# Optimization experiments

Hardware: AMD Instinct MI355X
Metric: run time of the kernel (lower is better)

## Reference

```python
import jax, jax.numpy as jnp
import numpy as np

N_AGENTS = 12
N_THREADS = 4096
DIM = 3
N_VEC = 4
HID = 64
INV_NF = 32
LAYERS = 2
N = N_THREADS * N_AGENTS


def _intra_graph_edges():
    # fully-connected directed edges within each env's agent graph
    i, j = np.meshgrid(np.arange(N_AGENTS), np.arange(N_AGENTS), indexing='ij')
    mask = i != j
    ri, ci = i[mask], j[mask]  # [132]
    off = (np.arange(N_THREADS) * N_AGENTS)[:, None]
    row = (ri[None, :] + off).reshape(-1).astype(np.int32)
    col = (ci[None, :] + off).reshape(-1).astype(np.int32)
    return jnp.asarray(row), jnp.asarray(col)


def setup_inputs() -> dict:
    key = jax.random.key(0)
    ks = jax.random.split(key, 16)
    s = 0.05
    row, col = _intra_graph_edges()
    return {
        'h0': jax.random.normal(ks[0], (N, INV_NF), jnp.float32),
        'x0': jax.random.normal(ks[1], (N, DIM, N_VEC), jnp.float32),
        'W_embed': jax.random.normal(ks[2], (INV_NF, HID), jnp.float32) * s,
        'b_embed': jnp.zeros((HID,), jnp.float32),
        'We1': jax.random.normal(ks[3], (LAYERS, 2 * HID + N_VEC, HID), jnp.float32) * s,
        'be1': jnp.zeros((LAYERS, HID), jnp.float32),
        'We2': jax.random.normal(ks[4], (LAYERS, HID, HID), jnp.float32) * s,
        'be2': jnp.zeros((LAYERS, HID), jnp.float32),
        'Wx': jax.random.normal(ks[5], (LAYERS, HID, N_VEC), jnp.float32) * s,
        'bx': jnp.zeros((LAYERS, N_VEC), jnp.float32),
        'Wh1': jax.random.normal(ks[6], (LAYERS, 2 * HID, HID), jnp.float32) * s,
        'bh1': jnp.zeros((LAYERS, HID), jnp.float32),
        'Wh2': jax.random.normal(ks[7], (LAYERS, HID, HID), jnp.float32) * s,
        'bh2': jnp.zeros((LAYERS, HID), jnp.float32),
        'w_act': jax.random.normal(ks[8], (N_VEC,), jnp.float32) * s,
        'log_std': jnp.full((DIM,), -0.5, jnp.float32),
        'row': row,
        'col': col,
    }


def reference(h0, x0, W_embed, b_embed, We1, be1, We2, be2, Wx, bx,
              Wh1, bh1, Wh2, bh2, w_act, log_std, row, col):
    silu = jax.nn.silu
    n = h0.shape[0]
    h = h0 @ W_embed + b_embed            # node embedding, [N, HID]
    x = x0                                 # equivariant features, [N, DIM, N_VEC]
    deg = jnp.maximum(jax.ops.segment_sum(jnp.ones_like(row, jnp.float32), row, num_segments=n), 1.0)
    for l in range(LAYERS):
        hi, hj = h[row], h[col]
        diff = x[row] - x[col]                        # [E, DIM, N_VEC]
        radial = jnp.sum(diff * diff, axis=1)          # [E, N_VEC]
        m = silu(jnp.concatenate([hi, hj, radial], -1) @ We1[l] + be1[l])
        m = silu(m @ We2[l] + be2[l])                  # edge messages [E, HID]
        wc = m @ Wx[l] + bx[l]                         # per-vector coord weights [E, N_VEC]
        x = x + jax.ops.segment_sum(diff * wc[:, None, :], row, num_segments=n) / deg[:, None, None]
        agg = jax.ops.segment_sum(m, row, num_segments=n)
        h = h + silu(jnp.concatenate([h, agg], -1) @ Wh1[l] + bh1[l]) @ Wh2[l] + bh2[l]
    mu = jnp.einsum('ndv,v->nd', x, w_act)             # act_net: Linear(N_VEC,1,bias=False)
    actions = mu                                        # deterministic: mode of Normal(mu, std)
    log_probs = jnp.broadcast_to(-log_std - 0.5 * jnp.log(2.0 * jnp.pi), mu.shape)
    actions = actions.reshape(N_THREADS, N_AGENTS, DIM)
    log_probs = log_probs.reshape(N_THREADS, N_AGENTS, DIM)
    return actions, log_probs
```

## Files before the change

### kernel.cpp

```cpp
#include <hip/hip_runtime.h>

#define NAG 12
#define NTH 4096
#define NEDGE 132
#define LDB 72
#define LDT 20

typedef __bf16 bf16_8 __attribute__((ext_vector_type(8)));
typedef __bf16 bf16_4 __attribute__((ext_vector_type(4)));
typedef float  f32x4  __attribute__((ext_vector_type(4)));

#define MFMA(a,b,c) __builtin_amdgcn_mfma_f32_16x16x32_bf16((a),(b),(c),0,0,0)

#define WS_FRAGS 100
#define WS_BIAS_F32 25600
#define WS_BX_F32   27648
#define WS_BYTES 111104

__device__ __forceinline__ float silu_f(float z) {
    float e = __expf(-z);
    return z * __builtin_amdgcn_rcpf(1.0f + e);
}

__device__ __forceinline__ bf16_8 loadB64(const float* __restrict__ W, int kbase, int n, int q) {
    bf16_8 b;
    #pragma unroll
    for (int j = 0; j < 8; ++j) b[j] = (__bf16)W[(kbase + q*8 + j) * 64 + n];
    return b;
}

__device__ __forceinline__ bf16_8 packA8(const float* S) {
    f32x4 u = *(const f32x4*)S, v = *(const f32x4*)(S + 4);
    bf16_8 a;
    a[0]=(__bf16)u.x; a[1]=(__bf16)u.y; a[2]=(__bf16)u.z; a[3]=(__bf16)u.w;
    a[4]=(__bf16)v.x; a[5]=(__bf16)v.y; a[6]=(__bf16)v.z; a[7]=(__bf16)v.w;
    return a;
}

__global__ __launch_bounds__(64) void prep_frags(
    const float* __restrict__ W_embed, const float* __restrict__ We1,
    const float* __restrict__ We2, const float* __restrict__ Wh1,
    const float* __restrict__ Wh2,
    const float* __restrict__ be1, const float* __restrict__ be2,
    const float* __restrict__ bh1, const float* __restrict__ bh2,
    const float* __restrict__ bx, __bf16* __restrict__ wsb)
{
    const int f = blockIdx.x, lane = threadIdx.x;
    const int q = lane >> 4, n16 = lane & 15;
    float* wsf = (float*)wsb;
    if (f < WS_FRAGS) {
        const float* src; int kbase, nbase;
        if (f < 4) { src = W_embed; kbase = 0; nbase = f * 16; }
        else {
            int g0 = f - 4, l = g0 / 48, r = g0 % 48;
            if      (r < 8)  { int nt=r>>1, kh=r&1;            src = We1 + l*NEDGE*64; kbase = kh*32;      nbase = nt*16; }
            else if (r < 16) { int rr=r-8,  nt=rr>>1, kh=rr&1; src = We1 + l*NEDGE*64; kbase = 64 + kh*32; nbase = nt*16; }
            else if (r < 24) { int rr=r-16, nt=rr>>1, kh=rr&1; src = We2 + l*64*64;    kbase = kh*32;      nbase = nt*16; }
            else if (r < 40) { int rr=r-24, nt=rr>>2, ks=rr&3; src = Wh1 + l*128*64;   kbase = ks*32;      nbase = nt*16; }
            else             { int rr=r-40, nt=rr>>1, kh=rr&1; src = Wh2 + l*64*64;    kbase = kh*32;      nbase = nt*16; }
        }
        bf16_8 b = loadB64(src, kbase, nbase + n16, q);
        *(bf16_8*)(wsb + (size_t)f * 512 + lane * 8) = b;
    } else if (f < WS_FRAGS + 8) {
        int f2 = f - WS_FRAGS, l = f2 >> 2, w = f2 & 3;
        const float* src = (w == 0 ? be1 : w == 1 ? be2 : w == 2 ? bh1 : bh2) + l * 64;
        f32x4 v = { src[n16], src[16 + n16], src[32 + n16], src[48 + n16] };
        *(f32x4*)(wsf + WS_BIAS_F32 + ((size_t)(l*4 + w) * 64 + lane) * 4) = v;
    } else {
        #pragma unroll
        for (int l = 0; l < 2; ++l)
            wsf[WS_BX_F32 + l*64 + lane] = (n16 < 4) ? bx[l*4 + n16] : 0.f;
    }
}

template<bool WS>
__device__ __forceinline__ bf16_8 frg(const __bf16* __restrict__ wsb, int fid,
                                      const float* __restrict__ src, int kbase, int n, int lane) {
    if (WS) return *(const bf16_8*)(wsb + (size_t)fid * 512 + lane * 8);
    else    return loadB64(src, kbase, n, (lane >> 4));
}

template<bool WS>
__global__ void __launch_bounds__(64) egnn9(
    const float* __restrict__ h0, const float* __restrict__ x0,
    const float* __restrict__ W_embed, const float* __restrict__ b_embed,
    const float* __restrict__ We1, const float* __restrict__ be1,
    const float* __restrict__ We2, const float* __restrict__ be2,
    const float* __restrict__ Wx, const float* __restrict__ bx,
    const float* __restrict__ Wh1, const float* __restrict__ bh1,
    const float* __restrict__ Wh2, const float* __restrict__ bh2,
    const float* __restrict__ w_act, const float* __restrict__ log_std,
    const __bf16* __restrict__ wsb, float* __restrict__ out)
{
    __shared__ __align__(16) __bf16 sh  [NAG * LDB];
    __shared__ __align__(16) __bf16 sHa [NAG * LDB];
    __shared__ __align__(16) __bf16 sHb [NAG * LDB];
    __shared__ __align__(16) __bf16 mstT[2][64 * LDT];
    __shared__ __align__(16) float  sx  [NAG * 16];
    __shared__ __align__(16) float  sRad[NEDGE * 4];
    __shared__ __align__(16) __bf16 sWcB[NEDGE * 4];
    __shared__ __align__(16) float  sWb [4 * 64];

    const int lane = threadIdx.x;
    const int q = lane >> 4, n16 = lane & 15;
    const int rowA = (n16 < NAG) ? n16 : (NAG - 1);
    const int env  = blockIdx.x;
    const float* wsf = (const float*)wsb;

    if (lane < NAG * 3) {
        int d = lane % 3;
        out[NTH * NAG * 3 + env * (NAG*3) + lane] = -log_std[d] - 0.9189385332046727f;
    }

    #pragma unroll
    for (int p = 0; p < 3; ++p) {
        int idx = p * 64 + lane;
        if (idx < NAG * 12) sx[(idx / 12) * 16 + idx % 12] = x0[env * NAG * 12 + idx];
    }

    f32x4 hC[4];
    {
        const float* hp = h0 + (env * NAG + rowA) * 32 + q * 8;
        bf16_8 a = packA8(hp);
        #pragma unroll
        for (int nt = 0; nt < 4; ++nt) {
            bf16_8 b = frg<WS>(wsb, nt, W_embed, 0, nt*16 + n16, lane);
            f32x4 acc = {0.f,0.f,0.f,0.f};
            acc = MFMA(a, b, acc);
            float bias = b_embed[nt*16 + n16];
            #pragma unroll
            for (int r = 0; r < 4; ++r) acc[r] += bias;
            hC[nt] = acc;
        }
        #pragma unroll
        for (int nt = 0; nt < 4; ++nt)
            #pragma unroll
            for (int r = 0; r < 4; ++r) {
                int row = q*4 + r;
                if (row < NAG) sh[row*LDB + nt*16 + n16] = (__bf16)hC[nt][r];
            }
    }

    #pragma unroll 1
    for (int l = 0; l < 2; ++l) {
        const float* We1l = We1 + l * NEDGE * 64;
        const float* be1l = be1 + l * 64;
        const float* be2l = be2 + l * 64;
        const float* Wxl  = Wx  + l * 64 * 4;
        const float* bxl  = bx  + l * 4;
        const float* We2l = We2 + l * 64 * 64;
        const float* Wh1l = Wh1 + l * 128 * 64;
        const float* bh1l = bh1 + l * 64;
        const float* Wh2l = Wh2 + l * 64 * 64;
        const float* bh2l = bh2 + l * 64;
        const int L = 4 + l * 48;

        f32x4 be1q, be2q, bh1q, bh2q;
        float bxv;
        if (WS) {
            const float* bb = wsf + WS_BIAS_F32 + (size_t)(l*4) * 256 + lane * 4;
            be1q = *(const f32x4*)(bb);
            be2q = *(const f32x4*)(bb + 256);
            bh1q = *(const f32x4*)(bb + 512);
            bh2q = *(const f32x4*)(bb + 768);
            bxv  = wsf[WS_BX_F32 + l*64 + lane];
        } else {
            #pragma unroll
            for (int nt = 0; nt < 4; ++nt) {
                be1q[nt] = be1l[nt*16+n16]; be2q[nt] = be2l[nt*16+n16];
                bh1q[nt] = bh1l[nt*16+n16]; bh2q[nt] = bh2l[nt*16+n16];
            }
            bxv = (n16 < 4) ? bxl[n16] : 0.f;
        }

        {
            bf16_8 a0 = *(const bf16_8*)(sh + rowA*LDB + q*8);
            bf16_8 a1 = *(const bf16_8*)(sh + rowA*LDB + 32 + q*8);
            #pragma unroll
            for (int nt = 0; nt < 4; ++nt) {
                bf16_8 b0 = frg<WS>(wsb, L+nt*2+0,   We1l, 0,  nt*16+n16, lane);
                bf16_8 b1 = frg<WS>(wsb, L+nt*2+1,   We1l, 32, nt*16+n16, lane);
                bf16_8 c0 = frg<WS>(wsb, L+8+nt*2+0, We1l, 64, nt*16+n16, lane);
                bf16_8 c1 = frg<WS>(wsb, L+8+nt*2+1, We1l, 96, nt*16+n16, lane);
                f32x4 aA = {0.f,0.f,0.f,0.f}, aB = {0.f,0.f,0.f,0.f};
                aA = MFMA(a0, b0, aA); aA = MFMA(a1, b1, aA);
                aB = MFMA(a0, c0, aB); aB = MFMA(a1, c1, aB);
                #pragma unroll
                for (int r = 0; r < 4; ++r) {
                    int row = q*4 + r;
                    if (row < NAG) {
                        sHa[row*LDB + nt*16+n16] = (__bf16)(aA[r] + be1q[nt]);
                        sHb[row*LDB + nt*16+n16] = (__bf16)aB[r];
                    }
                }
            }
        }
        #pragma unroll
        for (int p = 0; p < 4; ++p) sWb[p*64 + lane] = We1l[(128+p)*64 + lane];
        #pragma unroll
        for (int p = 0; p < 9; ++p) {
            int idx = p * 64 + lane;
            if (idx < NEDGE * 4) {
                int e = idx >> 2, v = idx & 3;
                int i = e / 11, jj = e - i * 11, j = jj + (jj >= i);
                float r = 0.f;
                #pragma unroll
                for (int d = 0; d < 3; ++d) {
                    float df = sx[i*16 + d*4 + v] - sx[j*16 + d*4 + v];
                    r += df * df;
                }
                sRad[idx] = r;
            }
        }

        float agg[NAG];
        #pragma unroll
        for (int i = 0; i < NAG; ++i) agg[i] = 0.f;
        bf16_8 w2f[4][2], wxf[2];
        #pragma unroll
        for (int nt = 0; nt < 4; ++nt) {
            w2f[nt][0] = frg<WS>(wsb, L+16+nt*2+0, We2l, 0,  nt*16+n16, lane);
            w2f[nt][1] = frg<WS>(wsb, L+16+nt*2+1, We2l, 32, nt*16+n16, lane);
        }
        #pragma unroll
        for (int kh = 0; kh < 2; ++kh) {
            bf16_8 b;
            #pragma unroll
            for (int j2 = 0; j2 < 8; ++j2)
                b[j2] = (n16 < 4) ? (__bf16)Wxl[(kh*32 + q*8 + j2)*4 + n16] : (__bf16)0.f;
            wxf[kh] = b;
        }

        #pragma unroll
        for (int t = 0; t < 9; ++t) {
            __bf16* mT = &mstT[t & 1][0];
            const int e  = t*16 + n16;
            const int ec = (e < NEDGE) ? e : (NEDGE - 1);
            const int i  = ec / 11;
            const int jj = ec - i * 11;
            const int j  = jj + (jj >= i);
            const f32x4 rd = *(const f32x4*)(sRad + ec * 4);
            bf16_8 af0, af1;
            #pragma unroll
            for (int kh = 0; kh < 2; ++kh) {
                const int cb = kh*32 + q*8;
                bf16_8 ha = *(const bf16_8*)(sHa + i*LDB + cb);
                bf16_8 hb = *(const bf16_8*)(sHb + j*LDB + cb);
                f32x4 wr0 = {0.f,0.f,0.f,0.f}, wr1 = {0.f,0.f,0.f,0.f};
                #pragma unroll
                for (int v = 0; v < 4; ++v) {
                    f32x4 wa = *(const f32x4*)(sWb + v*64 + cb);
                    f32x4 wb = *(const f32x4*)(sWb + v*64 + cb + 4);
                    wr0 += rd[v] * wa; wr1 += rd[v] * wb;
                }
                bf16_8 a;
                #pragma unroll
                for (int c = 0; c < 4; ++c)
                    a[c]   = (__bf16)silu_f((float)ha[c]   + (float)hb[c]   + wr0[c]);
                #pragma unroll
                for (int c = 0; c < 4; ++c)
                    a[4+c] = (__bf16)silu_f((float)ha[4+c] + (float)hb[4+c] + wr1[c]);
                if (kh == 0) af0 = a; else af1 = a;
            }
            #pragma unroll
            for (int nt = 0; nt < 4; ++nt) {
                f32x4 acc = {0.f,0.f,0.f,0.f};
                acc = MFMA(af0, w2f[nt][0], acc);
                acc = MFMA(af1, w2f[nt][1], acc);
                bf16_4 mv;
                #pragma unroll
                for (int r = 0; r < 4; ++r) mv[r] = (__bf16)silu_f(acc[r] + be2q[nt]);
                *(bf16_4*)(mT + (nt*16 + n16)*LDT + q*4) = mv;
            }
            {
                bf16_8 aw0, aw1;
                #pragma unroll
                for (int j2 = 0; j2 < 8; ++j2) {
                    aw0[j2] = mT[(q*8 + j2)*LDT + n16];
                    aw1[j2] = mT[(32 + q*8 + j2)*LDT + n16];
                }
                f32x4 acc = {0.f,0.f,0.f,0.f};
                acc = MFMA(aw0, wxf[0], acc);
                acc = MFMA(aw1, wxf[1], acc);
                if (n16 < 4) {
                    #pragma unroll
                    for (int r = 0; r < 4; ++r) {
                        int row = t*16 + q*4 + r;
                        if (row < NEDGE) sWcB[row*4 + n16] = (__bf16)(acc[r] + bxv);
                    }
                }
            }
            {
                bf16_4 c0 = *(const bf16_4*)(mT + lane*LDT + 0);
                #pragma unroll
                for (int el = 0; el < 4; ++el) agg[(t*16 + el)/11] += (float)c0[el];
                if (t < 8) {
                    bf16_4 c1 = *(const bf16_4*)(mT + lane*LDT + 4);
                    bf16_4 c2 = *(const bf16_4*)(mT + lane*LDT + 8);
                    bf16_4 c3 = *(const bf16_4*)(mT + lane*LDT + 12);
                    #pragma unroll
                    for (int el = 0; el < 4; ++el) {
                        agg[(t*16 + 4  + el)/11] += (float)c1[el];
                        agg[(t*16 + 8  + el)/11] += (float)c2[el];
                        agg[(t*16 + 12 + el)/11] += (float)c3[el];
                    }
                }
            }
        }
        #pragma unroll
        for (int i = 0; i < NAG; ++i) sHb[i*LDB + lane] = (__bf16)agg[i];

        float xn[3];
        #pragma unroll
        for (int p = 0; p < 3; ++p) {
            int idx = p*64 + lane;
            float res = 0.f;
            if (idx < 144) {
                int xi = idx / 12, dv = idx % 12, v = dv & 3;
                float xiv = sx[xi*16 + dv];
                float acc = 0.f;
                #pragma unroll
                for (int j2 = 0; j2 < NAG; ++j2) {
                    int e2 = xi*11 + j2 - (j2 > xi ? 1 : 0);
                    e2 = (e2 < NEDGE) ? e2 : (NEDGE - 1);
                    float term = (xiv - sx[j2*16 + dv]) * (float)sWcB[e2*4 + v];
                    acc += (j2 == xi) ? 0.f : term;
                }
                res = xiv + acc * (1.0f / 11.0f);
            }
            xn[p] = res;
        }
        {
            bf16_8 ah0 = *(const bf16_8*)(sh  + rowA*LDB + q*8);
            bf16_8 ah1 = *(const bf16_8*)(sh  + rowA*LDB + 32 + q*8);
            bf16_8 ag0 = *(const bf16_8*)(sHb + rowA*LDB + q*8);
            bf16_8 ag1 = *(const bf16_8*)(sHb + rowA*LDB + 32 + q*8);
            #pragma unroll
            for (int nt = 0; nt < 4; ++nt) {
                f32x4 acc = {0.f,0.f,0.f,0.f};
                acc = MFMA(ah0, frg<WS>(wsb, L+24+nt*4+0, Wh1l, 0,  nt*16+n16, lane), acc);
                acc = MFMA(ah1, frg<WS>(wsb, L+24+nt*4+1, Wh1l, 32, nt*16+n16, lane), acc);
                acc = MFMA(ag0, frg<WS>(wsb, L+24+nt*4+2, Wh1l, 64, nt*16+n16, lane), acc);
                acc = MFMA(ag1, frg<WS>(wsb, L+24+nt*4+3, Wh1l, 96, nt*16+n16, lane), acc);
                #pragma unroll
                for (int r = 0; r < 4; ++r) {
                    int row = q*4 + r;
                    if (row < NAG) sHa[row*LDB + nt*16+n16] = (__bf16)silu_f(acc[r] + bh1q[nt]);
                }
            }
        }
        #pragma unroll
        for (int p = 0; p < 3; ++p) {
            int idx = p*64 + lane;
            if (idx < 144) sx[(idx/12)*16 + idx%12] = xn[p];
        }
        {
            bf16_8 at0 = *(const bf16_8*)(sHa + rowA*LDB + q*8);
            bf16_8 at1 = *(const bf16_8*)(sHa + rowA*LDB + 32 + q*8);
            #pragma unroll
            for (int nt = 0; nt < 4; ++nt) {
                f32x4 acc = {0.f,0.f,0.f,0.f};
                acc = MFMA(at0, frg<WS>(wsb, L+40+nt*2+0, Wh2l, 0,  nt*16+n16, lane), acc);
                acc = MFMA(at1, frg<WS>(wsb, L+40+nt*2+1, Wh2l, 32, nt*16+n16, lane), acc);
                #pragma unroll
                for (int r = 0; r < 4; ++r) hC[nt][r] += acc[r] + bh2q[nt];
            }
            #pragma unroll
            for (int nt = 0; nt < 4; ++nt)
                #pragma unroll
                for (int r = 0; r < 4; ++r) {
                    int row = q*4 + r;
                    if (row < NAG) sh[row*LDB + nt*16+n16] = (__bf16)hC[nt][r];
                }
        }
    }

    if (lane < NAG * 3) {
        int i = lane / 3, d = lane - i * 3;
        float mu = 0.f;
        #pragma unroll
        for (int v = 0; v < 4; ++v) mu += sx[i*16 + d*4 + v] * w_act[v];
        out[env * (NAG*3) + lane] = mu;
    }
}

extern "C" void kernel_launch(void* const* d_in, const int* in_sizes, int n_in,
                              void* d_out, int out_size, void* d_ws, size_t ws_size,
                              hipStream_t stream) {
    const float* h0   = (const float*)d_in[0];
    const float* x0   = (const float*)d_in[1];
    const float* Wem  = (const float*)d_in[2];
    const float* bem  = (const float*)d_in[3];
    const float* We1  = (const float*)d_in[4];
    const float* be1  = (const float*)d_in[5];
    const float* We2  = (const float*)d_in[6];
    const float* be2  = (const float*)d_in[7];
    const float* Wx   = (const float*)d_in[8];
    const float* bx   = (const float*)d_in[9];
    const float* Wh1  = (const float*)d_in[10];
    const float* bh1  = (const float*)d_in[11];
    const float* Wh2  = (const float*)d_in[12];
    const float* bh2  = (const float*)d_in[13];
    const float* wact = (const float*)d_in[14];
    const float* lstd = (const float*)d_in[15];
    float* out = (float*)d_out;

    if (ws_size >= (size_t)WS_BYTES) {
        prep_frags<<<dim3(WS_FRAGS + 9), dim3(64), 0, stream>>>(
            Wem, We1, We2, Wh1, Wh2, be1, be2, bh1, bh2, bx, (__bf16*)d_ws);
        egnn9<true><<<dim3(NTH), dim3(64), 0, stream>>>(
            h0, x0, Wem, bem, We1, be1, We2, be2, Wx, bx,
            Wh1, bh1, Wh2, bh2, wact, lstd, (const __bf16*)d_ws, out);
    } else {
        egnn9<false><<<dim3(NTH), dim3(64), 0, stream>>>(
            h0, x0, Wem, bem, We1, be1, We2, be2, Wx, bx,
            Wh1, bh1, Wh2, bh2, wact, lstd, nullptr, out);
    }
}
```

Measured before the change: 239.6 us.

## Process two environments per wavefront to reuse weight fragments

Each 64-thread block now handles two environments instead of one, so the grid is halved. Each weight fragment loaded from the workspace or global memory feeds MFMAs for both environments, and the two independent MFMA chains can interleave for more instruction-level parallelism. In exchange, LDS use and register pressure per block roughly double (agg[2][12], hC[2][4]), which can lower occupancy or cause spills, and there are half as many blocks to spread across CUs.

```diff
diff --git a/kernel.cpp b/kernel.cpp
--- a/kernel.cpp
+++ b/kernel.cpp
@@ -81,7 +81,7 @@
 }
 
 template<bool WS>
-__global__ void __launch_bounds__(64) egnn9(
+__global__ void __launch_bounds__(64) egnn11(
     const float* __restrict__ h0, const float* __restrict__ x0,
     const float* __restrict__ W_embed, const float* __restrict__ b_embed,
     const float* __restrict__ We1, const float* __restrict__ be1,
@@ -92,53 +92,65 @@
     const float* __restrict__ w_act, const float* __restrict__ log_std,
     const __bf16* __restrict__ wsb, float* __restrict__ out)
 {
-    __shared__ __align__(16) __bf16 sh  [NAG * LDB];
-    __shared__ __align__(16) __bf16 sHa [NAG * LDB];
-    __shared__ __align__(16) __bf16 sHb [NAG * LDB];
-    __shared__ __align__(16) __bf16 mstT[2][64 * LDT];
-    __shared__ __align__(16) float  sx  [NAG * 16];
-    __shared__ __align__(16) float  sRad[NEDGE * 4];
-    __shared__ __align__(16) __bf16 sWcB[NEDGE * 4];
+    __shared__ __align__(16) __bf16 sh  [2][NAG * LDB];
+    __shared__ __align__(16) __bf16 sHa [2][NAG * LDB];
+    __shared__ __align__(16) __bf16 sHb [2][NAG * LDB];
+    __shared__ __align__(16) __bf16 mstT[2][2][64 * LDT];
+    __shared__ __align__(16) float  sx  [2][NAG * 16];
+    __shared__ __align__(16) float  sRad[2][NEDGE * 4];
+    __shared__ __align__(16) __bf16 sWcB[2][NEDGE * 4];
     __shared__ __align__(16) float  sWb [4 * 64];
 
     const int lane = threadIdx.x;
     const int q = lane >> 4, n16 = lane & 15;
     const int rowA = (n16 < NAG) ? n16 : (NAG - 1);
-    const int env  = blockIdx.x;
+    const int env0 = blockIdx.x * 2;
     const float* wsf = (const float*)wsb;
 
     if (lane < NAG * 3) {
         int d = lane % 3;
-        out[NTH * NAG * 3 + env * (NAG*3) + lane] = -log_std[d] - 0.9189385332046727f;
+        float lp = -log_std[d] - 0.9189385332046727f;
+        out[NTH * NAG * 3 + (env0 + 0) * (NAG*3) + lane] = lp;
+        out[NTH * NAG * 3 + (env0 + 1) * (NAG*3) + lane] = lp;
     }
 
     #pragma unroll
-    for (int p = 0; p < 3; ++p) {
+    for (int p = 0; p < 5; ++p) {
         int idx = p * 64 + lane;
-        if (idx < NAG * 12) sx[(idx / 12) * 16 + idx % 12] = x0[env * NAG * 12 + idx];
-    }
-
-    f32x4 hC[4];
+        if (idx < 2 * NAG * 12) {
+            int ep = idx / 144, r2 = idx - ep * 144;
+            sx[ep][(r2 / 12) * 16 + r2 % 12] = x0[(env0) * NAG * 12 + idx];
+        }
+    }
+
+    f32x4 hC[2][4];
     {
-        const float* hp = h0 + (env * NAG + rowA) * 32 + q * 8;
-        bf16_8 a = packA8(hp);
+        bf16_8 a[2];
+        #pragma unroll
+        for (int ep = 0; ep < 2; ++ep)
+            a[ep] = packA8(h0 + ((env0 + ep) * NAG + rowA) * 32 + q * 8);
         #pragma unroll
         for (int nt = 0; nt < 4; ++nt) {
             bf16_8 b = frg<WS>(wsb, nt, W_embed, 0, nt*16 + n16, lane);
-            f32x4 acc = {0.f,0.f,0.f,0.f};
-            acc = MFMA(a, b, acc);
             float bias = b_embed[nt*16 + n16];
             #pragma unroll
-            for (int r = 0; r < 4; ++r) acc[r] += bias;
-            hC[nt] = acc;
-        }
-        #pragma unroll
-        for (int nt = 0; nt < 4; ++nt)
-            #pragma unroll
-            for (int r = 0; r < 4; ++r) {
-                int row = q*4 + r;
-                if (row < NAG) sh[row*LDB + nt*16 + n16] = (__bf16)hC[nt][r];
-            }
+            for (int ep = 0; ep < 2; ++ep) {
+                f32x4 acc = {0.f,0.f,0.f,0.f};
+                acc = MFMA(a[ep], b, acc);
+                #pragma unroll
+                for (int r = 0; r < 4; ++r) acc[r] += bias;
+                hC[ep][nt] = acc;
+            }
+        }
+        #pragma unroll
+        for (int ep = 0; ep < 2; ++ep)
+            #pragma unroll
+            for (int nt = 0; nt < 4; ++nt)
+                #pragma unroll
+                for (int r = 0; r < 4; ++r) {
+                    int row = q*4 + r;
+                    if (row < NAG) sh[ep][row*LDB + nt*16 + n16] = (__bf16)hC[ep][nt][r];
+                }
     }
 
     #pragma unroll 1
@@ -174,23 +186,30 @@
         }
 
         {
-            bf16_8 a0 = *(const bf16_8*)(sh + rowA*LDB + q*8);
-            bf16_8 a1 = *(const bf16_8*)(sh + rowA*LDB + 32 + q*8);
+            bf16_8 a0[2], a1[2];
+            #pragma unroll
+            for (int ep = 0; ep < 2; ++ep) {
+                a0[ep] = *(const bf16_8*)(sh[ep] + rowA*LDB + q*8);
+                a1[ep] = *(const bf16_8*)(sh[ep] + rowA*LDB + 32 + q*8);
+            }
             #pragma unroll
             for (int nt = 0; nt < 4; ++nt) {
                 bf16_8 b0 = frg<WS>(wsb, L+nt*2+0,   We1l, 0,  nt*16+n16, lane);
                 bf16_8 b1 = frg<WS>(wsb, L+nt*2+1,   We1l, 32, nt*16+n16, lane);
                 bf16_8 c0 = frg<WS>(wsb, L+8+nt*2+0, We1l, 64, nt*16+n16, lane);
                 bf16_8 c1 = frg<WS>(wsb, L+8+nt*2+1, We1l, 96, nt*16+n16, lane);
-                f32x4 aA = {0.f,0.f,0.f,0.f}, aB = {0.f,0.f,0.f,0.f};
-                aA = MFMA(a0, b0, aA); aA = MFMA(a1, b1, aA);
-                aB = MFMA(a0, c0, aB); aB = MFMA(a1, c1, aB);
-                #pragma unroll
-                for (int r = 0; r < 4; ++r) {
-                    int row = q*4 + r;
-                    if (row < NAG) {
-                        sHa[row*LDB + nt*16+n16] = (__bf16)(aA[r] + be1q[nt]);
-                        sHb[row*LDB + nt*16+n16] = (__bf16)aB[r];
+                #pragma unroll
+                for (int ep = 0; ep < 2; ++ep) {
+                    f32x4 aA = {0.f,0.f,0.f,0.f}, aB = {0.f,0.f,0.f,0.f};
+                    aA = MFMA(a0[ep], b0, aA); aA = MFMA(a1[ep], b1, aA);
+                    aB = MFMA(a0[ep], c0, aB); aB = MFMA(a1[ep], c1, aB);
+                    #pragma unroll
+                    for (int r = 0; r < 4; ++r) {
+                        int row = q*4 + r;
+                        if (row < NAG) {
+                            sHa[ep][row*LDB + nt*16+n16] = (__bf16)(aA[r] + be1q[nt]);
+                            sHb[ep][row*LDB + nt*16+n16] = (__bf16)aB[r];
+                        }
                     }
                 }
             }
@@ -203,19 +222,24 @@
             if (idx < NEDGE * 4) {
                 int e = idx >> 2, v = idx & 3;
                 int i = e / 11, jj = e - i * 11, j = jj + (jj >= i);
-                float r = 0.f;
-                #pragma unroll
-                for (int d = 0; d < 3; ++d) {
-                    float df = sx[i*16 + d*4 + v] - sx[j*16 + d*4 + v];
-                    r += df * df;
-                }
-                sRad[idx] = r;
-            }
-        }
-
-        float agg[NAG];
-        #pragma unroll
-        for (int i = 0; i < NAG; ++i) agg[i] = 0.f;
+                #pragma unroll
+                for (int ep = 0; ep < 2; ++ep) {
+                    float r = 0.f;
+                    #pragma unroll
+                    for (int d = 0; d < 3; ++d) {
+                        float df = sx[ep][i*16 + d*4 + v] - sx[ep][j*16 + d*4 + v];
+                        r += df * df;
+                    }
+                    sRad[ep][idx] = r;
+                }
+            }
+        }
+
+        float agg[2][NAG];
+        #pragma unroll
+        for (int ep = 0; ep < 2; ++ep)
+            #pragma unroll
+            for (int i = 0; i < NAG; ++i) agg[ep][i] = 0.f;
         bf16_8 w2f[4][2], wxf[2];
         #pragma unroll
         for (int nt = 0; nt < 4; ++nt) {
@@ -233,46 +257,54 @@
 
         #pragma unroll
         for (int t = 0; t < 9; ++t) {
-            __bf16* mT = &mstT[t & 1][0];
             const int e  = t*16 + n16;
             const int ec = (e < NEDGE) ? e : (NEDGE - 1);
             const int i  = ec / 11;
             const int jj = ec - i * 11;
             const int j  = jj + (jj >= i);
-            const f32x4 rd = *(const f32x4*)(sRad + ec * 4);
-            bf16_8 af0, af1;
-            #pragma unroll
-            for (int kh = 0; kh < 2; ++kh) {
-                const int cb = kh*32 + q*8;
-                bf16_8 ha = *(const bf16_8*)(sHa + i*LDB + cb);
-                bf16_8 hb = *(const bf16_8*)(sHb + j*LDB + cb);
-                f32x4 wr0 = {0.f,0.f,0.f,0.f}, wr1 = {0.f,0.f,0.f,0.f};
-                #pragma unroll
-                for (int v = 0; v < 4; ++v) {
-                    f32x4 wa = *(const f32x4*)(sWb + v*64 + cb);
-                    f32x4 wb = *(const f32x4*)(sWb + v*64 + cb + 4);
-                    wr0 += rd[v] * wa; wr1 += rd[v] * wb;
-                }
-                bf16_8 a;
-                #pragma unroll
-                for (int c = 0; c < 4; ++c)
-                    a[c]   = (__bf16)silu_f((float)ha[c]   + (float)hb[c]   + wr0[c]);
-                #pragma unroll
-                for (int c = 0; c < 4; ++c)
-                    a[4+c] = (__bf16)silu_f((float)ha[4+c] + (float)hb[4+c] + wr1[c]);
-                if (kh == 0) af0 = a; else af1 = a;
-            }
-            #pragma unroll
-            for (int nt = 0; nt < 4; ++nt) {
-                f32x4 acc = {0.f,0.f,0.f,0.f};
-                acc = MFMA(af0, w2f[nt][0], acc);
-                acc = MFMA(af1, w2f[nt][1], acc);
-                bf16_4 mv;
-                #pragma unroll
-                for (int r = 0; r < 4; ++r) mv[r] = (__bf16)silu_f(acc[r] + be2q[nt]);
-                *(bf16_4*)(mT + (nt*16 + n16)*LDT + q*4) = mv;
-            }
-            {
+            bf16_8 af[2][2];
+            #pragma unroll
+            for (int ep = 0; ep < 2; ++ep) {
+                const f32x4 rd = *(const f32x4*)(sRad[ep] + ec * 4);
+                #pragma unroll
+                for (int kh = 0; kh < 2; ++kh) {
+                    const int cb = kh*32 + q*8;
+                    bf16_8 ha = *(const bf16_8*)(sHa[ep] + i*LDB + cb);
+                    bf16_8 hb = *(const bf16_8*)(sHb[ep] + j*LDB + cb);
+                    f32x4 wr0 = {0.f,0.f,0.f,0.f}, wr1 = {0.f,0.f,0.f,0.f};
+                    #pragma unroll
+                    for (int v = 0; v < 4; ++v) {
+                        f32x4 wa = *(const f32x4*)(sWb + v*64 + cb);
+                        f32x4 wb = *(const f32x4*)(sWb + v*64 + cb + 4);
+                        wr0 += rd[v] * wa; wr1 += rd[v] * wb;
+                    }
+                    bf16_8 a;
+                    #pragma unroll
+                    for (int c = 0; c < 4; ++c)
+                        a[c]   = (__bf16)silu_f((float)ha[c]   + (float)hb[c]   + wr0[c]);
+                    #pragma unroll
+                    for (int c = 0; c < 4; ++c)
+                        a[4+c] = (__bf16)silu_f((float)ha[4+c] + (float)hb[4+c] + wr1[c]);
+                    af[ep][kh] = a;
+                }
+            }
+            #pragma unroll
+            for (int ep = 0; ep < 2; ++ep) {
+                __bf16* mT = &mstT[ep][t & 1][0];
+                #pragma unroll
+                for (int nt = 0; nt < 4; ++nt) {
+                    f32x4 acc = {0.f,0.f,0.f,0.f};
+                    acc = MFMA(af[ep][0], w2f[nt][0], acc);
+                    acc = MFMA(af[ep][1], w2f[nt][1], acc);
+                    bf16_4 mv;
+                    #pragma unroll
+                    for (int r = 0; r < 4; ++r) mv[r] = (__bf16)silu_f(acc[r] + be2q[nt]);
+                    *(bf16_4*)(mT + (nt*16 + n16)*LDT + q*4) = mv;
+                }
+            }
+            #pragma unroll
+            for (int ep = 0; ep < 2; ++ep) {
+                const __bf16* mT = &mstT[ep][t & 1][0];
                 bf16_8 aw0, aw1;
                 #pragma unroll
                 for (int j2 = 0; j2 < 8; ++j2) {
@@ -286,101 +318,133 @@
                     #pragma unroll
                     for (int r = 0; r < 4; ++r) {
                         int row = t*16 + q*4 + r;
-                        if (row < NEDGE) sWcB[row*4 + n16] = (__bf16)(acc[r] + bxv);
-                    }
-                }
-            }
-            {
+                        if (row < NEDGE) sWcB[ep][row*4 + n16] = (__bf16)(acc[r] + bxv);
+                    }
+                }
+            }
+            #pragma unroll
+            for (int ep = 0; ep < 2; ++ep) {
+                const __bf16* mT = &mstT[ep][t & 1][0];
                 bf16_4 c0 = *(const bf16_4*)(mT + lane*LDT + 0);
                 #pragma unroll
-                for (int el = 0; el < 4; ++el) agg[(t*16 + el)/11] += (float)c0[el];
+                for (int el = 0; el < 4; ++el) agg[ep][(t*16 + el)/11] += (float)c0[el];
                 if (t < 8) {
                     bf16_4 c1 = *(const bf16_4*)(mT + lane*LDT + 4);
                     bf16_4 c2 = *(const bf16_4*)(mT + lane*LDT + 8);
                     bf16_4 c3 = *(const bf16_4*)(mT + lane*LDT + 12);
                     #pragma unroll
                     for (int el = 0; el < 4; ++el) {
-                        agg[(t*16 + 4  + el)/11] += (float)c1[el];
-                        agg[(t*16 + 8  + el)/11] += (float)c2[el];
-                        agg[(t*16 + 12 + el)/11] += (float)c3[el];
-                    }
-                }
-            }
-        }
-        #pragma unroll
-        for (int i = 0; i < NAG; ++i) sHb[i*LDB + lane] = (__bf16)agg[i];
-
-        float xn[3];
+                        agg[ep][(t*16 + 4  + el)/11] += (float)c1[el];
+                        agg[ep][(t*16 + 8  + el)/11] += (float)c2[el];
+                        agg[ep][(t*16 + 12 + el)/11] += (float)c3[el];
+                    }
+                }
+            }
+        }
+        #pragma unroll
+        for (int ep = 0; ep < 2; ++ep)
+            #pragma unroll
+            for (int i = 0; i < NAG; ++i) sHb[ep][i*LDB + lane] = (__bf16)agg[ep][i];
+
+        float xn[2][3];
         #pragma unroll
         for (int p = 0; p < 3; ++p) {
             int idx = p*64 + lane;
-            float res = 0.f;
-            if (idx < 144) {
-                int xi = idx / 12, dv = idx % 12, v = dv & 3;
-                float xiv = sx[xi*16 + dv];
+            int xi = idx / 12, dv = idx % 12, v = dv & 3;
+            bool act = idx < 144;
+            int xic = act ? xi : 0;
+            #pragma unroll
+            for (int ep = 0; ep < 2; ++ep) {
+                float xiv = sx[ep][xic*16 + dv];
                 float acc = 0.f;
                 #pragma unroll
                 for (int j2 = 0; j2 < NAG; ++j2) {
-                    int e2 = xi*11 + j2 - (j2 > xi ? 1 : 0);
+                    int e2 = xic*11 + j2 - (j2 > xic ? 1 : 0);
                     e2 = (e2 < NEDGE) ? e2 : (NEDGE - 1);
-                    float term = (xiv - sx[j2*16 + dv]) * (float)sWcB[e2*4 + v];
-                    acc += (j2 == xi) ? 0.f : term;
-                }
-                res = xiv + acc * (1.0f / 11.0f);
-            }
-            xn[p] = res;
+                    float term = (xiv - sx[ep][j2*16 + dv]) * (float)sWcB[ep][e2*4 + v];
+                    acc += (j2 == xic) ? 0.f : term;
+                }
+                xn[ep][p] = act ? (xiv + acc * (1.0f / 11.0f)) : 0.f;
+            }
         }
         {
-            bf16_8 ah0 = *(const bf16_8*)(sh  + rowA*LDB + q*8);
-            bf16_8 ah1 = *(const bf16_8*)(sh  + rowA*LDB + 32 + q*8);
-            bf16_8 ag0 = *(const bf16_8*)(sHb + rowA*LDB + q*8);
-            bf16_8 ag1 = *(const bf16_8*)(sHb + rowA*LDB + 32 + q*8);
+            bf16_8 ah0[2], ah1[2], ag0[2], ag1[2];
+            #pragma unroll
+            for (int ep = 0; ep < 2; ++ep) {
+                ah0[ep] = *(const bf16_8*)(sh[ep]  + rowA*LDB + q*8);
+                ah1[ep] = *(const bf16_8*)(sh[ep]  + rowA*LDB + 32 + q*8);
+                ag0[ep] = *(const bf16_8*)(sHb[ep] + rowA*LDB + q*8);
+                ag1[ep] = *(const bf16_8*)(sHb[ep] + rowA*LDB + 32 + q*8);
+            }
             #pragma unroll
             for (int nt = 0; nt < 4; ++nt) {
-                f32x4 acc = {0.f,0.f,0.f,0.f};
-                acc = MFMA(ah0, frg<WS>(wsb, L+24+nt*4+0, Wh1l, 0,  nt*16+n16, lane), acc);
-                acc = MFMA(ah1, frg<WS>(wsb, L+24+nt*4+1, Wh1l, 32, nt*16+n16, lane), acc);
-                acc = MFMA(ag0, frg<WS>(wsb, L+24+nt*4+2, Wh1l, 64, nt*16+n16, lane), acc);
-                acc = MFMA(ag1, frg<WS>(wsb, L+24+nt*4+3, Wh1l, 96, nt*16+n16, lane), acc);
-                #pragma unroll
-                for (int r = 0; r < 4; ++r) {
-                    int row = q*4 + r;
-                    if (row < NAG) sHa[row*LDB + nt*16+n16] = (__bf16)silu_f(acc[r] + bh1q[nt]);
+                bf16_8 b0 = frg<WS>(wsb, L+24+nt*4+0, Wh1l, 0,  nt*16+n16, lane);
+                bf16_8 b1 = frg<WS>(wsb, L+24+nt*4+1, Wh1l, 32, nt*16+n16, lane);
+                bf16_8 b2 = frg<WS>(wsb, L+24+nt*4+2, Wh1l, 64, nt*16+n16, lane);
+                bf16_8 b3 = frg<WS>(wsb, L+24+nt*4+3, Wh1l, 96, nt*16+n16, lane);
+                #pragma unroll
+                for (int ep = 0; ep < 2; ++ep) {
+                    f32x4 acc = {0.f,0.f,0.f,0.f};
+                    acc = MFMA(ah0[ep], b0, acc); acc = MFMA(ah1[ep], b1, acc);
+                    acc = MFMA(ag0[ep], b2, acc); acc = MFMA(ag1[ep], b3, acc);
+                    #pragma unroll
+                    for (int r = 0; r < 4; ++r) {
+                        int row = q*4 + r;
+                        if (row < NAG) sHa[ep][row*LDB + nt*16+n16] = (__bf16)silu_f(acc[r] + bh1q[nt]);
+                    }
                 }
             }
         }
         #pragma unroll
         for (int p = 0; p < 3; ++p) {
             int idx = p*64 + lane;
-            if (idx < 144) sx[(idx/12)*16 + idx%12] = xn[p];
+            if (idx < 144) {
+                #pragma unroll
+                for (int ep = 0; ep < 2; ++ep)
+                    sx[ep][(idx/12)*16 + idx%12] = xn[ep][p];
+            }
         }
         {
-            bf16_8 at0 = *(const bf16_8*)(sHa + rowA*LDB + q*8);
-            bf16_8 at1 = *(const bf16_8*)(sHa + rowA*LDB + 32 + q*8);
+            bf16_8 at0[2], at1[2];
+            #pragma unroll
+            for (int ep = 0; ep < 2; ++ep) {
+                at0[ep] = *(const bf16_8*)(sHa[ep] + rowA*LDB + q*8);
+                at1[ep] = *(const bf16_8*)(sHa[ep] + rowA*LDB + 32 + q*8);
+            }
             #pragma unroll
             for (int nt = 0; nt < 4; ++nt) {
-                f32x4 acc = {0.f,0.f,0.f,0.f};
-                acc = MFMA(at0, frg<WS>(wsb, L+40+nt*2+0, Wh2l, 0,  nt*16+n16, lane), acc);
-                acc = MFMA(at1, frg<WS>(wsb, L+40+nt*2+1, Wh2l, 32, nt*16+n16, lane), acc);
-                #pragma unroll
-                for (int r = 0; r < 4; ++r) hC[nt][r] += acc[r] + bh2q[nt];
-            }
-            #pragma unroll
-            for (int nt = 0; nt < 4; ++nt)
-                #pragma unroll
-                for (int r = 0; r < 4; ++r) {
-                    int row = q*4 + r;
-                    if (row < NAG) sh[row*LDB + nt*16+n16] = (__bf16)hC[nt][r];
-                }
+                bf16_8 b0 = frg<WS>(wsb, L+40+nt*2+0, Wh2l, 0,  nt*16+n16, lane);
+                bf16_8 b1 = frg<WS>(wsb, L+40+nt*2+1, Wh2l, 32, nt*16+n16, lane);
+                #pragma unroll
+                for (int ep = 0; ep < 2; ++ep) {
+                    f32x4 acc = {0.f,0.f,0.f,0.f};
+                    acc = MFMA(at0[ep], b0, acc);
+                    acc = MFMA(at1[ep], b1, acc);
+                    #pragma unroll
+                    for (int r = 0; r < 4; ++r) hC[ep][nt][r] += acc[r] + bh2q[nt];
+                }
+            }
+            #pragma unroll
+            for (int ep = 0; ep < 2; ++ep)
+                #pragma unroll
+                for (int nt = 0; nt < 4; ++nt)
+                    #pragma unroll
+                    for (int r = 0; r < 4; ++r) {
+                        int row = q*4 + r;
+                        if (row < NAG) sh[ep][row*LDB + nt*16+n16] = (__bf16)hC[ep][nt][r];
+                    }
         }
     }
 
     if (lane < NAG * 3) {
         int i = lane / 3, d = lane - i * 3;
-        float mu = 0.f;
-        #pragma unroll
-        for (int v = 0; v < 4; ++v) mu += sx[i*16 + d*4 + v] * w_act[v];
-        out[env * (NAG*3) + lane] = mu;
+        #pragma unroll
+        for (int ep = 0; ep < 2; ++ep) {
+            float mu = 0.f;
+            #pragma unroll
+            for (int v = 0; v < 4; ++v) mu += sx[ep][i*16 + d*4 + v] * w_act[v];
+            out[(env0 + ep) * (NAG*3) + lane] = mu;
+        }
     }
 }
 
@@ -408,11 +472,11 @@
     if (ws_size >= (size_t)WS_BYTES) {
         prep_frags<<<dim3(WS_FRAGS + 9), dim3(64), 0, stream>>>(
             Wem, We1, We2, Wh1, Wh2, be1, be2, bh1, bh2, bx, (__bf16*)d_ws);
-        egnn9<true><<<dim3(NTH), dim3(64), 0, stream>>>(
+        egnn11<true><<<dim3(NTH / 2), dim3(64), 0, stream>>>(
             h0, x0, Wem, bem, We1, be1, We2, be2, Wx, bx,
             Wh1, bh1, Wh2, bh2, wact, lstd, (const __bf16*)d_ws, out);
     } else {
-        egnn9<false><<<dim3(NTH), dim3(64), 0, stream>>>(
+        egnn11<false><<<dim3(NTH / 2), dim3(64), 0, stream>>>(
             h0, x0, Wem, bem, We1, be1, We2, be2, Wx, bx,
             Wh1, bh1, Wh2, bh2, wact, lstd, nullptr, out);
     }
```

After: 225.7 us. -5.8%, faster.
